# Kernel optimization log

Hardware: AMD Instinct MI355X
Metric: run time of the kernel (lower is better)

## Reference

```python
import jax, jax.numpy as jnp
import numpy as np

IN, H, B, T, OUT = 128, 512, 256, 512, 2

def _lstm_layer(x, Wih, Whh, bih, bhh):
    # x: [B, T, D_in] -> h_seq: [B, T, H]. PyTorch gate order: i, f, g, o.
    gx = jnp.einsum('btd,gd->btg', x, Wih) + bih + bhh  # [B, T, 4H]
    gx = jnp.transpose(gx, (1, 0, 2))                    # [T, B, 4H]
    Hh = Whh.shape[1]
    def step(carry, g_t):
        h, c = carry
        g = g_t + h @ Whh.T
        i = jax.nn.sigmoid(g[:, 0*Hh:1*Hh])
        f = jax.nn.sigmoid(g[:, 1*Hh:2*Hh])
        gg = jnp.tanh(g[:, 2*Hh:3*Hh])
        o = jax.nn.sigmoid(g[:, 3*Hh:4*Hh])
        c = f * c + i * gg
        h = o * jnp.tanh(c)
        return (h, c), h
    h0 = jnp.zeros((x.shape[0], Hh), x.dtype)
    (_, _), hs = jax.lax.scan(step, (h0, h0), gx)
    return jnp.transpose(hs, (1, 0, 2))  # [B, T, H]

def setup_inputs() -> dict:
    key = jax.random.key(0)
    ks = jax.random.split(key, 11)
    s = 1.0 / np.sqrt(H)
    u = lambda k, shp: jax.random.uniform(k, shp, jnp.float32, -s, s)
    return {
        'x':    jax.random.normal(ks[0], (B, T, IN), jnp.float32),
        'Wih0': u(ks[1], (4 * H, IN)), 'Whh0': u(ks[2], (4 * H, H)),
        'bih0': u(ks[3], (4 * H,)),    'bhh0': u(ks[4], (4 * H,)),
        'Wih1': u(ks[5], (4 * H, H)),  'Whh1': u(ks[6], (4 * H, H)),
        'bih1': u(ks[7], (4 * H,)),    'bhh1': u(ks[8], (4 * H,)),
        'Wfc':  u(ks[9], (OUT, H)),    'bfc':  u(ks[10], (OUT,)),
    }

def reference(x, Wih0, Whh0, bih0, bhh0, Wih1, Whh1, bih1, bhh1, Wfc, bfc):
    h1 = _lstm_layer(x, Wih0, Whh0, bih0, bhh0)   # layer 0
    h2 = _lstm_layer(h1, Wih1, Whh1, bih1, bhh1)  # layer 1
    return h2[:, -1, :] @ Wfc.T + bfc             # [B, OUT]
```

## Files before the change

### kernel.cpp

```cpp
#include <hip/hip_runtime.h>

#define IN_DIM 128
#define HID    512
#define BATCH  256
#define SEQT   512
#define G4H    2048
#define K0     640
#define K1     1024
#define NC0    20
#define NC1    32
#define ACOLS  1152
#define ROWB   2304

typedef __attribute__((ext_vector_type(8))) short bf16x8;
typedef __attribute__((ext_vector_type(4))) float f32x4;

#define MFMA16 __builtin_amdgcn_mfma_f32_16x16x32_bf16

__device__ __forceinline__ unsigned short f2bf(float f) {
  unsigned u = __float_as_uint(f);
  u += 0x7fffu + ((u >> 16) & 1u);
  return (unsigned short)(u >> 16);
}
__device__ __forceinline__ float bf2f(unsigned short s) {
  return __uint_as_float(((unsigned)s) << 16);
}
__device__ __forceinline__ float sigm(float x) { return 1.0f / (1.0f + __expf(-x)); }
__device__ __forceinline__ float tanh_f(float x) {
  float xc = fminf(fmaxf(x, -15.0f), 15.0f);
  float e = __expf(2.0f * xc);
  return (e - 1.0f) / (e + 1.0f);
}

__device__ __forceinline__ unsigned ald(const unsigned* p) {
  return __hip_atomic_load(p, __ATOMIC_RELAXED, __HIP_MEMORY_SCOPE_AGENT);
}

__global__ void conv_weights(const float* __restrict__ Wih0, const float* __restrict__ Whh0,
                             const float* __restrict__ Wih1, const float* __restrict__ Whh1,
                             const float* __restrict__ bih0, const float* __restrict__ bhh0,
                             const float* __restrict__ bih1, const float* __restrict__ bhh1,
                             short* __restrict__ W0h, short* __restrict__ W0l,
                             short* __restrict__ W1h, short* __restrict__ W1l,
                             float* __restrict__ bsum0, float* __restrict__ bsum1) {
  int idx = blockIdx.x * blockDim.x + threadIdx.x;
  const int N0 = G4H * K0, N1 = G4H * K1;
  if (idx < N0) {
    int tile = idx / (K0 * 16), rem = idx % (K0 * 16);
    int kcg = rem >> 9, l = (rem >> 3) & 63, j = rem & 7;
    int slice = tile >> 2, g = tile & 3;
    int c = l & 15, k = kcg * 32 + ((l >> 4) << 3) + j;
    int n = g * HID + slice * 16 + c;
    float w = (k < IN_DIM) ? Wih0[n * IN_DIM + k] : Whh0[n * HID + (k - IN_DIM)];
    unsigned short hi = f2bf(w);
    W0h[idx] = (short)hi;
    W0l[idx] = (short)f2bf(w - bf2f(hi));
  } else if (idx < N0 + N1) {
    int d = idx - N0;
    int tile = d / (K1 * 16), rem = d % (K1 * 16);
    int kcg = rem >> 9, l = (rem >> 3) & 63, j = rem & 7;
    int slice = tile >> 2, g = tile & 3;
    int c = l & 15, k = kcg * 32 + ((l >> 4) << 3) + j;
    int n = g * HID + slice * 16 + c;
    float w = (k < HID) ? Wih1[n * HID + k] : Whh1[n * HID + (k - HID)];
    unsigned short hi = f2bf(w);
    W1h[d] = (short)hi;
    W1l[d] = (short)f2bf(w - bf2f(hi));
  } else if (idx < N0 + N1 + G4H) {
    int n = idx - (N0 + N1);
    bsum0[n] = bih0[n] + bhh0[n];
  } else if (idx < N0 + N1 + 2 * G4H) {
    int n = idx - (N0 + N1 + G4H);
    bsum1[n] = bih1[n] + bhh1[n];
  }
}

__device__ __forceinline__ void stage_both(char* AhiB, char* AloB,
                                           const unsigned* __restrict__ h0p,
                                           const unsigned* __restrict__ h2p,
                                           int b0, int tid) {
  const int row = tid >> 5, c32 = tid & 31;
  const unsigned* p0 = h0p + (size_t)(b0 + row) * HID + c32 * 16;
  const unsigned* p2 = h2p + (size_t)(b0 + row) * HID + c32 * 16;
  uint4 v0, v1, v2, v3, w0, w1, w2, w3;
  asm volatile(
      "global_load_dwordx4 %0, %8, off sc0 sc1\n\t"
      "global_load_dwordx4 %1, %8, off offset:16 sc0 sc1\n\t"
      "global_load_dwordx4 %2, %8, off offset:32 sc0 sc1\n\t"
      "global_load_dwordx4 %3, %8, off offset:48 sc0 sc1\n\t"
      "global_load_dwordx4 %4, %9, off sc0 sc1\n\t"
      "global_load_dwordx4 %5, %9, off offset:16 sc0 sc1\n\t"
      "global_load_dwordx4 %6, %9, off offset:32 sc0 sc1\n\t"
      "global_load_dwordx4 %7, %9, off offset:48 sc0 sc1\n\t"
      "s_waitcnt vmcnt(0)"
      : "=&v"(v0), "=&v"(v1), "=&v"(v2), "=&v"(v3),
        "=&v"(w0), "=&v"(w1), "=&v"(w2), "=&v"(w3)
      : "v"(p0), "v"(p2)
      : "memory");

  const int rx = (row & 7) << 4;
  char* bh = AhiB + row * ROWB;
  char* bl = AloB + row * ROWB;
#define PKH(a, b) ((unsigned)((a) & 0xffffu) | (((b) & 0xffffu) << 16))
#define PKL(a, b) (((a) >> 16) | ((b) & 0xffff0000u))
  {
    const int byte0 = (IN_DIM + c32 * 16) * 2;
    int4 h0 = {(int)PKH(v0.x, v0.y), (int)PKH(v0.z, v0.w), (int)PKH(v1.x, v1.y), (int)PKH(v1.z, v1.w)};
    int4 h1 = {(int)PKH(v2.x, v2.y), (int)PKH(v2.z, v2.w), (int)PKH(v3.x, v3.y), (int)PKH(v3.z, v3.w)};
    int4 l0 = {(int)PKL(v0.x, v0.y), (int)PKL(v0.z, v0.w), (int)PKL(v1.x, v1.y), (int)PKL(v1.z, v1.w)};
    int4 l1 = {(int)PKL(v2.x, v2.y), (int)PKL(v2.z, v2.w), (int)PKL(v3.x, v3.y), (int)PKL(v3.z, v3.w)};
    *(int4*)(bh + (byte0 ^ rx)) = h0;
    *(int4*)(bh + ((byte0 + 16) ^ rx)) = h1;
    *(int4*)(bl + (byte0 ^ rx)) = l0;
    *(int4*)(bl + ((byte0 + 16) ^ rx)) = l1;
  }
  {
    const int byte0 = (IN_DIM + HID + c32 * 16) * 2;
    int4 h0 = {(int)PKH(w0.x, w0.y), (int)PKH(w0.z, w0.w), (int)PKH(w1.x, w1.y), (int)PKH(w1.z, w1.w)};
    int4 h1 = {(int)PKH(w2.x, w2.y), (int)PKH(w2.z, w2.w), (int)PKH(w3.x, w3.y), (int)PKH(w3.z, w3.w)};
    int4 l0 = {(int)PKL(w0.x, w0.y), (int)PKL(w0.z, w0.w), (int)PKL(w1.x, w1.y), (int)PKL(w1.z, w1.w)};
    int4 l1 = {(int)PKL(w2.x, w2.y), (int)PKL(w2.z, w2.w), (int)PKL(w3.x, w3.y), (int)PKL(w3.z, w3.w)};
    *(int4*)(bh + (byte0 ^ rx)) = h0;
    *(int4*)(bh + ((byte0 + 16) ^ rx)) = h1;
    *(int4*)(bl + (byte0 ^ rx)) = l0;
    *(int4*)(bl + ((byte0 + 16) ^ rx)) = l1;
  }
#undef PKH
#undef PKL
}

template <int NKC>
__device__ __forceinline__ void gemmq(const char* Ah, const char* Al,
                                      const short* __restrict__ Bh, const short* __restrict__ Bl,
                                      int lane, int aoff, f32x4& acc0, f32x4& acc1) {
  const int row = lane & 15;
  const int ko  = (lane >> 4) * 8;
  const int rx  = (row & 7) << 4;
  const char* pAh0 = Ah + row * ROWB;
  const char* pAh1 = Ah + (row + 16) * ROWB;
  const char* pAl0 = Al + row * ROWB;
  const char* pAl1 = Al + (row + 16) * ROWB;
#pragma unroll
  for (int kc = 0; kc < NKC; ++kc) {
    const int off = ((aoff + kc * 32 + ko) * 2) ^ rx;
    bf16x8 ah0 = *(const bf16x8*)(pAh0 + off);
    bf16x8 ah1 = *(const bf16x8*)(pAh1 + off);
    bf16x8 al0 = *(const bf16x8*)(pAl0 + off);
    bf16x8 al1 = *(const bf16x8*)(pAl1 + off);
    bf16x8 bh  = *(const bf16x8*)(Bh + kc * 512 + lane * 8);
    bf16x8 bl  = *(const bf16x8*)(Bl + kc * 512 + lane * 8);
    acc0 = MFMA16(ah0, bh, acc0, 0, 0, 0);
    acc1 = MFMA16(ah1, bh, acc1, 0, 0, 0);
    acc0 = MFMA16(ah0, bl, acc0, 0, 0, 0);
    acc1 = MFMA16(ah1, bl, acc1, 0, 0, 0);
    acc0 = MFMA16(al0, bh, acc0, 0, 0, 0);
    acc1 = MFMA16(al1, bh, acc1, 0, 0, 0);
  }
}

__device__ __forceinline__ void finq(float* glf, int g, int lane,
                                     const f32x4& a0, const f32x4& a1) {
  const int col = lane & 15;
  const int r0  = (lane >> 4) * 4;
  float* base = glf + g * 512;
#pragma unroll
  for (int r = 0; r < 4; ++r) {
    atomicAdd(base + (r0 + r) * 16 + col, a0[r]);
    atomicAdd(base + (16 + r0 + r) * 16 + col, a1[r]);
  }
}

__device__ __forceinline__ void do_update(float* glf, float& c, const float* bs,
                                          int tid, unsigned (*hbuf)[16]) {
  float gi = glf[tid]        + bs[0];
  float gf = glf[512 + tid]  + bs[1];
  float gg = glf[1024 + tid] + bs[2];
  float go = glf[1536 + tid] + bs[3];
  glf[tid] = 0.f; glf[512 + tid] = 0.f; glf[1024 + tid] = 0.f; glf[1536 + tid] = 0.f;
  float i = sigm(gi), f = sigm(gf), g = tanh_f(gg), o = sigm(go);
  float cc = f * c + i * g;
  c = cc;
  float h = o * tanh_f(cc);
  unsigned short hh = f2bf(h);
  unsigned short hl = f2bf(h - bf2f(hh));
  hbuf[tid >> 4][tid & 15] = (unsigned)hh | ((unsigned)hl << 16);
}

__device__ __forceinline__ void store_h(const unsigned (*hbuf)[16], unsigned* hc,
                                        int b0, int hid0, int tid) {
  if (tid < 128) {
    const int row = tid >> 2, q = tid & 3;
    const unsigned long long* src = (const unsigned long long*)&hbuf[row][q * 4];
    unsigned long long* dst =
        (unsigned long long*)(hc + (size_t)(b0 + row) * HID + hid0 + q * 4);
    __hip_atomic_store(dst, src[0], __ATOMIC_RELAXED, __HIP_MEMORY_SCOPE_AGENT);
    __hip_atomic_store(dst + 1, src[1], __ATOMIC_RELAXED, __HIP_MEMORY_SCOPE_AGENT);
  }
}

__device__ __forceinline__ void group_barrier(unsigned* cnt, unsigned target, int tid) {
  asm volatile("s_waitcnt vmcnt(0)" ::: "memory");
  __syncthreads();
  if (tid == 0) {
    __hip_atomic_fetch_add(cnt, 1u, __ATOMIC_RELAXED, __HIP_MEMORY_SCOPE_AGENT);
    while (__hip_atomic_load(cnt, __ATOMIC_RELAXED, __HIP_MEMORY_SCOPE_AGENT) < target)
      __builtin_amdgcn_s_sleep(1);
  }
  __syncthreads();
}

__global__ void __launch_bounds__(1024, 4) lstm_fused(
    const float* __restrict__ x,
    const float* __restrict__ Wfc, const float* __restrict__ bfc,
    const short* __restrict__ W0h, const short* __restrict__ W0l,
    const short* __restrict__ W1h, const short* __restrict__ W1l,
    const float* __restrict__ bsum0, const float* __restrict__ bsum1,
    unsigned* __restrict__ h0s, unsigned* __restrict__ h2s,
    unsigned* __restrict__ counters,
    float* __restrict__ out) {
  const int tid   = threadIdx.x;
  const int wv    = tid >> 6;
  const int lane  = tid & 63;
  const int slice = blockIdx.x & 31;
  const int grp   = blockIdx.x >> 5;
  const int hid0  = slice * 16;
  const int b0    = grp * 32;
  unsigned* cnt   = counters + grp * 64;

  __shared__ __align__(16) char AhiB[32 * ROWB];
  __shared__ __align__(16) char AloB[32 * ROWB];
  __shared__ float glf[4 * 512];
  __shared__ __align__(16) unsigned hbuf[32][16];

  const int g  = wv & 3;
  const int kq = wv >> 2;
  const short* B0hp = W0h + ((size_t)(slice * 4 + g) * NC0 + (size_t)kq * 5) * 512;
  const short* B0lp = W0l + ((size_t)(slice * 4 + g) * NC0 + (size_t)kq * 5) * 512;
  const short* B1hp = W1h + ((size_t)(slice * 4 + g) * NC1 + (size_t)kq * 8) * 512;
  const short* B1lp = W1l + ((size_t)(slice * 4 + g) * NC1 + (size_t)kq * 8) * 512;
  const int aoff0 = kq * 160;
  const int aoff1 = IN_DIM + kq * 256;

  float c0 = 0.f, c1 = 0.f;
  float bs0[4], bs1[4];
  if (tid < 512) {
    const int n = hid0 + (tid & 15);
#pragma unroll
    for (int q = 0; q < 4; ++q) { bs0[q] = bsum0[q * HID + n]; bs1[q] = bsum1[q * HID + n]; }
    glf[tid] = 0.f; glf[512 + tid] = 0.f; glf[1024 + tid] = 0.f; glf[1536 + tid] = 0.f;
  }

  const size_t PL = (size_t)BATCH * HID;

  for (int s = 0; s <= SEQT; ++s) {
    const int cur = s & 1, prv = cur ^ 1;
    unsigned* h0c = h0s + (size_t)cur * PL;
    const unsigned* h0p = h0s + (size_t)prv * PL;
    unsigned* h2c = h2s + (size_t)cur * PL;
    const unsigned* h2p = h2s + (size_t)prv * PL;

    if (s < SEQT) {
      const int row = tid >> 5, t32 = tid & 31;
      const int rx = (row & 7) << 4;
      const float* xs = x + ((size_t)(b0 + row) * SEQT + s) * IN_DIM + t32 * 4;
      float4 xv = *(const float4*)xs;
      unsigned short h0v = f2bf(xv.x), h1v = f2bf(xv.y), h2v = f2bf(xv.z), h3v = f2bf(xv.w);
      uint2 hd = {(unsigned)h0v | ((unsigned)h1v << 16), (unsigned)h2v | ((unsigned)h3v << 16)};
      uint2 ld = {(unsigned)f2bf(xv.x - bf2f(h0v)) | ((unsigned)f2bf(xv.y - bf2f(h1v)) << 16),
                  (unsigned)f2bf(xv.z - bf2f(h2v)) | ((unsigned)f2bf(xv.w - bf2f(h3v)) << 16)};
      const int byte = (t32 * 8) ^ rx;
      *(uint2*)(AhiB + row * ROWB + byte) = hd;
      *(uint2*)(AloB + row * ROWB + byte) = ld;
    }
    stage_both(AhiB, AloB, h0p, h2p, b0, tid);
    __syncthreads();

    if (s < SEQT) {
      f32x4 a0 = {0.f, 0.f, 0.f, 0.f}, a1 = {0.f, 0.f, 0.f, 0.f};
      gemmq<5>(AhiB, AloB, B0hp, B0lp, lane, aoff0, a0, a1);
      finq(glf, g, lane, a0, a1);
    }
    __syncthreads();
    if (s < SEQT && tid < 512) do_update(glf, c0, bs0, tid, hbuf);
    __syncthreads();

    if (s < SEQT) store_h(hbuf, h0c, b0, hid0, tid);
    if (s > 0) {
      f32x4 a0 = {0.f, 0.f, 0.f, 0.f}, a1 = {0.f, 0.f, 0.f, 0.f};
      gemmq<8>(AhiB, AloB, B1hp, B1lp, lane, aoff1, a0, a1);
      finq(glf, g, lane, a0, a1);
    }
    __syncthreads();
    if (s > 0 && tid < 512) do_update(glf, c1, bs1, tid, hbuf);
    __syncthreads();
    if (s > 0) store_h(hbuf, h2c, b0, hid0, tid);

    group_barrier(cnt, 32u * (unsigned)(s + 1), tid);
  }

  {
    const int p = tid >> 3, q = tid & 7;
    float acc = 0.f;
    if (slice == 0 && tid < 512) {
      const int b = b0 + (p >> 1), o = p & 1;
      const unsigned* sp = h2s + (size_t)b * HID + q * 64;
      const float* wf = Wfc + (size_t)o * HID + q * 64;
#pragma unroll 8
      for (int i = 0; i < 64; ++i) {
        unsigned u = ald(sp + i);
        acc += (bf2f((unsigned short)(u & 0xffff)) + bf2f((unsigned short)(u >> 16))) * wf[i];
      }
      glf[p * 8 + q] = acc;
    }
    __syncthreads();
    if (slice == 0 && tid < 512 && q == 0) {
      float t = 0.f;
#pragma unroll
      for (int i = 0; i < 8; ++i) t += glf[p * 8 + i];
      out[(b0 + (p >> 1)) * 2 + (p & 1)] = t + bfc[p & 1];
    }
  }
}

extern "C" void kernel_launch(void* const* d_in, const int* in_sizes, int n_in,
                              void* d_out, int out_size, void* d_ws, size_t ws_size,
                              hipStream_t stream) {
  const float* x    = (const float*)d_in[0];
  const float* Wih0 = (const float*)d_in[1];
  const float* Whh0 = (const float*)d_in[2];
  const float* bih0 = (const float*)d_in[3];
  const float* bhh0 = (const float*)d_in[4];
  const float* Wih1 = (const float*)d_in[5];
  const float* Whh1 = (const float*)d_in[6];
  const float* bih1 = (const float*)d_in[7];
  const float* bhh1 = (const float*)d_in[8];
  const float* Wfc  = (const float*)d_in[9];
  const float* bfc  = (const float*)d_in[10];
  float* out = (float*)d_out;

  short* W0h = (short*)d_ws;
  short* W0l = W0h + (size_t)G4H * K0;
  short* W1h = W0l + (size_t)G4H * K0;
  short* W1l = W1h + (size_t)G4H * K1;
  unsigned* h0s = (unsigned*)(W1l + (size_t)G4H * K1);
  unsigned* h2s = h0s + (size_t)2 * BATCH * HID;
  unsigned* counters = h2s + (size_t)2 * BATCH * HID;
  float* bsum0 = (float*)(counters + 512);
  float* bsum1 = bsum0 + G4H;

  (void)hipMemsetAsync(h0s, 0,
                       (size_t)4 * BATCH * HID * sizeof(unsigned) + 512 * sizeof(unsigned),
                       stream);

  const int total = G4H * K0 + G4H * K1 + 2 * G4H;
  conv_weights<<<(total + 255) / 256, 256, 0, stream>>>(
      Wih0, Whh0, Wih1, Whh1, bih0, bhh0, bih1, bhh1,
      W0h, W0l, W1h, W1l, bsum0, bsum1);

  void* args[] = {(void*)&x,    (void*)&Wfc,  (void*)&bfc,
                  (void*)&W0h,  (void*)&W0l,  (void*)&W1h, (void*)&W1l,
                  (void*)&bsum0, (void*)&bsum1,
                  (void*)&h0s,  (void*)&h2s,  (void*)&counters, (void*)&out};
  (void)hipLaunchCooperativeKernel((void*)lstm_fused, dim3(256), dim3(1024), args, 0,
                                   stream);
}
```

Baseline: 16.85 ms.

## Split workgroups by LSTM layer so both layers' steps run concurrently

Each workgroup now owns one layer (role from block index) and 32 hidden units, instead of computing both layers serially for 16 units. Per time step this drops from five block barriers with two GEMM/update phases to three barriers with one phase. The GEMM computes two 16-column tiles per wave. The gate buffer gets a padded [row][gate][col] layout, and h is stored directly to global without an LDS staging buffer. The cost is a heavier per-wave MFMA load for the layer-1 role, which now sets the per-step critical path.

```diff
diff --git a/kernel.cpp b/kernel.cpp
--- a/kernel.cpp
+++ b/kernel.cpp
@@ -9,13 +9,13 @@
 #define K1     1024
 #define NC0    20
 #define NC1    32
-#define ACOLS  1152
-#define ROWB   2304
+#define ROWB   2048
 
 typedef __attribute__((ext_vector_type(8))) short bf16x8;
 typedef __attribute__((ext_vector_type(4))) float f32x4;
 
 #define MFMA16 __builtin_amdgcn_mfma_f32_16x16x32_bf16
+#define GL(r, g, c) ((r) * 132 + (g) * 33 + (c))
 
 __device__ __forceinline__ unsigned short f2bf(float f) {
   unsigned u = __float_as_uint(f);
@@ -75,13 +75,48 @@
   }
 }
 
-__device__ __forceinline__ void stage_both(char* AhiB, char* AloB,
-                                           const unsigned* __restrict__ h0p,
-                                           const unsigned* __restrict__ h2p,
-                                           int b0, int tid) {
+#define PKH(a, b) ((unsigned)((a) & 0xffffu) | (((b) & 0xffffu) << 16))
+#define PKL(a, b) (((a) >> 16) | ((b) & 0xffff0000u))
+
+__device__ __forceinline__ void unpack16(char* bh, char* bl, int byte0, int rx,
+                                         const uint4& v0, const uint4& v1,
+                                         const uint4& v2, const uint4& v3) {
+  int4 h0 = {(int)PKH(v0.x, v0.y), (int)PKH(v0.z, v0.w), (int)PKH(v1.x, v1.y), (int)PKH(v1.z, v1.w)};
+  int4 h1 = {(int)PKH(v2.x, v2.y), (int)PKH(v2.z, v2.w), (int)PKH(v3.x, v3.y), (int)PKH(v3.z, v3.w)};
+  int4 l0 = {(int)PKL(v0.x, v0.y), (int)PKL(v0.z, v0.w), (int)PKL(v1.x, v1.y), (int)PKL(v1.z, v1.w)};
+  int4 l1 = {(int)PKL(v2.x, v2.y), (int)PKL(v2.z, v2.w), (int)PKL(v3.x, v3.y), (int)PKL(v3.z, v3.w)};
+  *(int4*)(bh + (byte0 ^ rx)) = h0;
+  *(int4*)(bh + ((byte0 + 16) ^ rx)) = h1;
+  *(int4*)(bl + (byte0 ^ rx)) = l0;
+  *(int4*)(bl + ((byte0 + 16) ^ rx)) = l1;
+}
+
+__device__ __forceinline__ void stage_one(char* AhiB, char* AloB,
+                                          const unsigned* __restrict__ plane,
+                                          int b0, int colOff, int tid) {
   const int row = tid >> 5, c32 = tid & 31;
-  const unsigned* p0 = h0p + (size_t)(b0 + row) * HID + c32 * 16;
-  const unsigned* p2 = h2p + (size_t)(b0 + row) * HID + c32 * 16;
+  const unsigned* p = plane + (size_t)(b0 + row) * HID + c32 * 16;
+  uint4 v0, v1, v2, v3;
+  asm volatile(
+      "global_load_dwordx4 %0, %4, off sc0 sc1\n\t"
+      "global_load_dwordx4 %1, %4, off offset:16 sc0 sc1\n\t"
+      "global_load_dwordx4 %2, %4, off offset:32 sc0 sc1\n\t"
+      "global_load_dwordx4 %3, %4, off offset:48 sc0 sc1\n\t"
+      "s_waitcnt vmcnt(0)"
+      : "=&v"(v0), "=&v"(v1), "=&v"(v2), "=&v"(v3)
+      : "v"(p)
+      : "memory");
+  const int rx = (row & 7) << 4;
+  unpack16(AhiB + row * ROWB, AloB + row * ROWB, (colOff + c32 * 16) * 2, rx, v0, v1, v2, v3);
+}
+
+__device__ __forceinline__ void stage_two(char* AhiB, char* AloB,
+                                          const unsigned* __restrict__ pA,
+                                          const unsigned* __restrict__ pB,
+                                          int b0, int tid) {
+  const int row = tid >> 5, c32 = tid & 31;
+  const unsigned* p0 = pA + (size_t)(b0 + row) * HID + c32 * 16;
+  const unsigned* p2 = pB + (size_t)(b0 + row) * HID + c32 * 16;
   uint4 v0, v1, v2, v3, w0, w1, w2, w3;
   asm volatile(
       "global_load_dwordx4 %0, %8, off sc0 sc1\n\t"
@@ -97,42 +132,21 @@
         "=&v"(w0), "=&v"(w1), "=&v"(w2), "=&v"(w3)
       : "v"(p0), "v"(p2)
       : "memory");
-
   const int rx = (row & 7) << 4;
   char* bh = AhiB + row * ROWB;
   char* bl = AloB + row * ROWB;
-#define PKH(a, b) ((unsigned)((a) & 0xffffu) | (((b) & 0xffffu) << 16))
-#define PKL(a, b) (((a) >> 16) | ((b) & 0xffff0000u))
-  {
-    const int byte0 = (IN_DIM + c32 * 16) * 2;
-    int4 h0 = {(int)PKH(v0.x, v0.y), (int)PKH(v0.z, v0.w), (int)PKH(v1.x, v1.y), (int)PKH(v1.z, v1.w)};
-    int4 h1 = {(int)PKH(v2.x, v2.y), (int)PKH(v2.z, v2.w), (int)PKH(v3.x, v3.y), (int)PKH(v3.z, v3.w)};
-    int4 l0 = {(int)PKL(v0.x, v0.y), (int)PKL(v0.z, v0.w), (int)PKL(v1.x, v1.y), (int)PKL(v1.z, v1.w)};
-    int4 l1 = {(int)PKL(v2.x, v2.y), (int)PKL(v2.z, v2.w), (int)PKL(v3.x, v3.y), (int)PKL(v3.z, v3.w)};
-    *(int4*)(bh + (byte0 ^ rx)) = h0;
-    *(int4*)(bh + ((byte0 + 16) ^ rx)) = h1;
-    *(int4*)(bl + (byte0 ^ rx)) = l0;
-    *(int4*)(bl + ((byte0 + 16) ^ rx)) = l1;
-  }
-  {
-    const int byte0 = (IN_DIM + HID + c32 * 16) * 2;
-    int4 h0 = {(int)PKH(w0.x, w0.y), (int)PKH(w0.z, w0.w), (int)PKH(w1.x, w1.y), (int)PKH(w1.z, w1.w)};
-    int4 h1 = {(int)PKH(w2.x, w2.y), (int)PKH(w2.z, w2.w), (int)PKH(w3.x, w3.y), (int)PKH(w3.z, w3.w)};
-    int4 l0 = {(int)PKL(w0.x, w0.y), (int)PKL(w0.z, w0.w), (int)PKL(w1.x, w1.y), (int)PKL(w1.z, w1.w)};
-    int4 l1 = {(int)PKL(w2.x, w2.y), (int)PKL(w2.z, w2.w), (int)PKL(w3.x, w3.y), (int)PKL(w3.z, w3.w)};
-    *(int4*)(bh + (byte0 ^ rx)) = h0;
-    *(int4*)(bh + ((byte0 + 16) ^ rx)) = h1;
-    *(int4*)(bl + (byte0 ^ rx)) = l0;
-    *(int4*)(bl + ((byte0 + 16) ^ rx)) = l1;
-  }
+  unpack16(bh, bl, (c32 * 16) * 2, rx, v0, v1, v2, v3);
+  unpack16(bh, bl, (HID + c32 * 16) * 2, rx, w0, w1, w2, w3);
+}
 #undef PKH
 #undef PKL
-}
 
 template <int NKC>
-__device__ __forceinline__ void gemmq(const char* Ah, const char* Al,
-                                      const short* __restrict__ Bh, const short* __restrict__ Bl,
-                                      int lane, int aoff, f32x4& acc0, f32x4& acc1) {
+__device__ __forceinline__ void gemm32(const char* Ah, const char* Al,
+                                       const short* __restrict__ Bh0, const short* __restrict__ Bl0,
+                                       const short* __restrict__ Bh1, const short* __restrict__ Bl1,
+                                       int lane, int aoff,
+                                       f32x4& a00, f32x4& a01, f32x4& a10, f32x4& a11) {
   const int row = lane & 15;
   const int ko  = (lane >> 4) * 8;
   const int rx  = (row & 7) << 4;
@@ -147,54 +161,36 @@
     bf16x8 ah1 = *(const bf16x8*)(pAh1 + off);
     bf16x8 al0 = *(const bf16x8*)(pAl0 + off);
     bf16x8 al1 = *(const bf16x8*)(pAl1 + off);
-    bf16x8 bh  = *(const bf16x8*)(Bh + kc * 512 + lane * 8);
-    bf16x8 bl  = *(const bf16x8*)(Bl + kc * 512 + lane * 8);
-    acc0 = MFMA16(ah0, bh, acc0, 0, 0, 0);
-    acc1 = MFMA16(ah1, bh, acc1, 0, 0, 0);
-    acc0 = MFMA16(ah0, bl, acc0, 0, 0, 0);
-    acc1 = MFMA16(ah1, bl, acc1, 0, 0, 0);
-    acc0 = MFMA16(al0, bh, acc0, 0, 0, 0);
-    acc1 = MFMA16(al1, bh, acc1, 0, 0, 0);
-  }
-}
-
-__device__ __forceinline__ void finq(float* glf, int g, int lane,
-                                     const f32x4& a0, const f32x4& a1) {
+    bf16x8 bh0 = *(const bf16x8*)(Bh0 + kc * 512 + lane * 8);
+    bf16x8 bl0 = *(const bf16x8*)(Bl0 + kc * 512 + lane * 8);
+    bf16x8 bh1 = *(const bf16x8*)(Bh1 + kc * 512 + lane * 8);
+    bf16x8 bl1 = *(const bf16x8*)(Bl1 + kc * 512 + lane * 8);
+    a00 = MFMA16(ah0, bh0, a00, 0, 0, 0);
+    a01 = MFMA16(ah1, bh0, a01, 0, 0, 0);
+    a00 = MFMA16(ah0, bl0, a00, 0, 0, 0);
+    a01 = MFMA16(ah1, bl0, a01, 0, 0, 0);
+    a00 = MFMA16(al0, bh0, a00, 0, 0, 0);
+    a01 = MFMA16(al1, bh0, a01, 0, 0, 0);
+    a10 = MFMA16(ah0, bh1, a10, 0, 0, 0);
+    a11 = MFMA16(ah1, bh1, a11, 0, 0, 0);
+    a10 = MFMA16(ah0, bl1, a10, 0, 0, 0);
+    a11 = MFMA16(ah1, bl1, a11, 0, 0, 0);
+    a10 = MFMA16(al0, bh1, a10, 0, 0, 0);
+    a11 = MFMA16(al1, bh1, a11, 0, 0, 0);
+  }
+}
+
+__device__ __forceinline__ void finq32(float* glf, int g, int lane,
+                                       const f32x4& a00, const f32x4& a01,
+                                       const f32x4& a10, const f32x4& a11) {
   const int col = lane & 15;
   const int r0  = (lane >> 4) * 4;
-  float* base = glf + g * 512;
 #pragma unroll
   for (int r = 0; r < 4; ++r) {
-    atomicAdd(base + (r0 + r) * 16 + col, a0[r]);
-    atomicAdd(base + (16 + r0 + r) * 16 + col, a1[r]);
-  }
-}
-
-__device__ __forceinline__ void do_update(float* glf, float& c, const float* bs,
-                                          int tid, unsigned (*hbuf)[16]) {
-  float gi = glf[tid]        + bs[0];
-  float gf = glf[512 + tid]  + bs[1];
-  float gg = glf[1024 + tid] + bs[2];
-  float go = glf[1536 + tid] + bs[3];
-  glf[tid] = 0.f; glf[512 + tid] = 0.f; glf[1024 + tid] = 0.f; glf[1536 + tid] = 0.f;
-  float i = sigm(gi), f = sigm(gf), g = tanh_f(gg), o = sigm(go);
-  float cc = f * c + i * g;
-  c = cc;
-  float h = o * tanh_f(cc);
-  unsigned short hh = f2bf(h);
-  unsigned short hl = f2bf(h - bf2f(hh));
-  hbuf[tid >> 4][tid & 15] = (unsigned)hh | ((unsigned)hl << 16);
-}
-
-__device__ __forceinline__ void store_h(const unsigned (*hbuf)[16], unsigned* hc,
-                                        int b0, int hid0, int tid) {
-  if (tid < 128) {
-    const int row = tid >> 2, q = tid & 3;
-    const unsigned long long* src = (const unsigned long long*)&hbuf[row][q * 4];
-    unsigned long long* dst =
-        (unsigned long long*)(hc + (size_t)(b0 + row) * HID + hid0 + q * 4);
-    __hip_atomic_store(dst, src[0], __ATOMIC_RELAXED, __HIP_MEMORY_SCOPE_AGENT);
-    __hip_atomic_store(dst + 1, src[1], __ATOMIC_RELAXED, __HIP_MEMORY_SCOPE_AGENT);
+    atomicAdd(glf + GL(r0 + r, g, col), a00[r]);
+    atomicAdd(glf + GL(16 + r0 + r, g, col), a01[r]);
+    atomicAdd(glf + GL(r0 + r, g, col + 16), a10[r]);
+    atomicAdd(glf + GL(16 + r0 + r, g, col + 16), a11[r]);
   }
 }
 
@@ -218,37 +214,49 @@
     unsigned* __restrict__ h0s, unsigned* __restrict__ h2s,
     unsigned* __restrict__ counters,
     float* __restrict__ out) {
-  const int tid   = threadIdx.x;
-  const int wv    = tid >> 6;
-  const int lane  = tid & 63;
-  const int slice = blockIdx.x & 31;
-  const int grp   = blockIdx.x >> 5;
-  const int hid0  = slice * 16;
-  const int b0    = grp * 32;
-  unsigned* cnt   = counters + grp * 64;
+  const int tid  = threadIdx.x;
+  const int wv   = tid >> 6;
+  const int lane = tid & 63;
+  const int wid  = blockIdx.x & 31;
+  const int grp  = blockIdx.x >> 5;
+  const int role = wid >> 4;
+  const int w16  = wid & 15;
+  const int hid0 = w16 * 32;
+  const int b0   = grp * 32;
+  unsigned* cnt  = counters + grp * 64;
 
   __shared__ __align__(16) char AhiB[32 * ROWB];
   __shared__ __align__(16) char AloB[32 * ROWB];
-  __shared__ float glf[4 * 512];
-  __shared__ __align__(16) unsigned hbuf[32][16];
+  __shared__ float glf[32 * 132];
 
   const int g  = wv & 3;
   const int kq = wv >> 2;
-  const short* B0hp = W0h + ((size_t)(slice * 4 + g) * NC0 + (size_t)kq * 5) * 512;
-  const short* B0lp = W0l + ((size_t)(slice * 4 + g) * NC0 + (size_t)kq * 5) * 512;
-  const short* B1hp = W1h + ((size_t)(slice * 4 + g) * NC1 + (size_t)kq * 8) * 512;
-  const short* B1lp = W1l + ((size_t)(slice * 4 + g) * NC1 + (size_t)kq * 8) * 512;
-  const int aoff0 = kq * 160;
-  const int aoff1 = IN_DIM + kq * 256;
-
-  float c0 = 0.f, c1 = 0.f;
-  float bs0[4], bs1[4];
-  if (tid < 512) {
-    const int n = hid0 + (tid & 15);
+  const int t0 = (w16 * 2) * 4 + g, t1 = t0 + 4;
+  const short *Bh0, *Bl0, *Bh1, *Bl1;
+  int aoff;
+  if (role == 0) {
+    Bh0 = W0h + ((size_t)t0 * NC0 + (size_t)kq * 5) * 512;
+    Bl0 = W0l + ((size_t)t0 * NC0 + (size_t)kq * 5) * 512;
+    Bh1 = W0h + ((size_t)t1 * NC0 + (size_t)kq * 5) * 512;
+    Bl1 = W0l + ((size_t)t1 * NC0 + (size_t)kq * 5) * 512;
+    aoff = kq * 160;
+  } else {
+    Bh0 = W1h + ((size_t)t0 * NC1 + (size_t)kq * 8) * 512;
+    Bl0 = W1l + ((size_t)t0 * NC1 + (size_t)kq * 8) * 512;
+    Bh1 = W1h + ((size_t)t1 * NC1 + (size_t)kq * 8) * 512;
+    Bl1 = W1l + ((size_t)t1 * NC1 + (size_t)kq * 8) * 512;
+    aoff = kq * 256;
+  }
+
+  float c = 0.f;
+  float bs[4];
+  {
+    const int n = hid0 + (tid & 31);
+    const float* bsp = role ? bsum1 : bsum0;
 #pragma unroll
-    for (int q = 0; q < 4; ++q) { bs0[q] = bsum0[q * HID + n]; bs1[q] = bsum1[q * HID + n]; }
-    glf[tid] = 0.f; glf[512 + tid] = 0.f; glf[1024 + tid] = 0.f; glf[1536 + tid] = 0.f;
-  }
+    for (int q = 0; q < 4; ++q) bs[q] = bsp[q * HID + n];
+  }
+  for (int i = tid; i < 32 * 132; i += 1024) glf[i] = 0.f;
 
   const size_t PL = (size_t)BATCH * HID;
 
@@ -258,42 +266,60 @@
     const unsigned* h0p = h0s + (size_t)prv * PL;
     unsigned* h2c = h2s + (size_t)cur * PL;
     const unsigned* h2p = h2s + (size_t)prv * PL;
-
-    if (s < SEQT) {
-      const int row = tid >> 5, t32 = tid & 31;
-      const int rx = (row & 7) << 4;
-      const float* xs = x + ((size_t)(b0 + row) * SEQT + s) * IN_DIM + t32 * 4;
-      float4 xv = *(const float4*)xs;
-      unsigned short h0v = f2bf(xv.x), h1v = f2bf(xv.y), h2v = f2bf(xv.z), h3v = f2bf(xv.w);
-      uint2 hd = {(unsigned)h0v | ((unsigned)h1v << 16), (unsigned)h2v | ((unsigned)h3v << 16)};
-      uint2 ld = {(unsigned)f2bf(xv.x - bf2f(h0v)) | ((unsigned)f2bf(xv.y - bf2f(h1v)) << 16),
-                  (unsigned)f2bf(xv.z - bf2f(h2v)) | ((unsigned)f2bf(xv.w - bf2f(h3v)) << 16)};
-      const int byte = (t32 * 8) ^ rx;
-      *(uint2*)(AhiB + row * ROWB + byte) = hd;
-      *(uint2*)(AloB + row * ROWB + byte) = ld;
-    }
-    stage_both(AhiB, AloB, h0p, h2p, b0, tid);
+    const bool active = role ? (s > 0) : (s < SEQT);
+
+    if (active) {
+      if (role == 0) {
+        {
+          const int row = tid >> 5, t32 = tid & 31;
+          const int rx = (row & 7) << 4;
+          const float* xs = x + ((size_t)(b0 + row) * SEQT + s) * IN_DIM + t32 * 4;
+          float4 xv = *(const float4*)xs;
+          unsigned short h0v = f2bf(xv.x), h1v = f2bf(xv.y), h2v = f2bf(xv.z), h3v = f2bf(xv.w);
+          uint2 hd = {(unsigned)h0v | ((unsigned)h1v << 16), (unsigned)h2v | ((unsigned)h3v << 16)};
+          uint2 ld = {(unsigned)f2bf(xv.x - bf2f(h0v)) | ((unsigned)f2bf(xv.y - bf2f(h1v)) << 16),
+                      (unsigned)f2bf(xv.z - bf2f(h2v)) | ((unsigned)f2bf(xv.w - bf2f(h3v)) << 16)};
+          const int byte = (t32 * 8) ^ rx;
+          *(uint2*)(AhiB + row * ROWB + byte) = hd;
+          *(uint2*)(AloB + row * ROWB + byte) = ld;
+        }
+        stage_one(AhiB, AloB, h0p, b0, IN_DIM, tid);
+      } else {
+        stage_two(AhiB, AloB, h0p, h2p, b0, tid);
+      }
+    }
     __syncthreads();
 
-    if (s < SEQT) {
-      f32x4 a0 = {0.f, 0.f, 0.f, 0.f}, a1 = {0.f, 0.f, 0.f, 0.f};
-      gemmq<5>(AhiB, AloB, B0hp, B0lp, lane, aoff0, a0, a1);
-      finq(glf, g, lane, a0, a1);
+    if (active) {
+      f32x4 a00 = {0.f, 0.f, 0.f, 0.f}, a01 = {0.f, 0.f, 0.f, 0.f};
+      f32x4 a10 = {0.f, 0.f, 0.f, 0.f}, a11 = {0.f, 0.f, 0.f, 0.f};
+      if (role == 0)
+        gemm32<5>(AhiB, AloB, Bh0, Bl0, Bh1, Bl1, lane, aoff, a00, a01, a10, a11);
+      else
+        gemm32<8>(AhiB, AloB, Bh0, Bl0, Bh1, Bl1, lane, aoff, a00, a01, a10, a11);
+      finq32(glf, g, lane, a00, a01, a10, a11);
     }
     __syncthreads();
-    if (s < SEQT && tid < 512) do_update(glf, c0, bs0, tid, hbuf);
-    __syncthreads();
-
-    if (s < SEQT) store_h(hbuf, h0c, b0, hid0, tid);
-    if (s > 0) {
-      f32x4 a0 = {0.f, 0.f, 0.f, 0.f}, a1 = {0.f, 0.f, 0.f, 0.f};
-      gemmq<8>(AhiB, AloB, B1hp, B1lp, lane, aoff1, a0, a1);
-      finq(glf, g, lane, a0, a1);
-    }
-    __syncthreads();
-    if (s > 0 && tid < 512) do_update(glf, c1, bs1, tid, hbuf);
-    __syncthreads();
-    if (s > 0) store_h(hbuf, h2c, b0, hid0, tid);
+
+    if (active) {
+      const int row = tid >> 5, col = tid & 31;
+      float gi = glf[GL(row, 0, col)] + bs[0];
+      float gf = glf[GL(row, 1, col)] + bs[1];
+      float gg = glf[GL(row, 2, col)] + bs[2];
+      float go = glf[GL(row, 3, col)] + bs[3];
+      glf[GL(row, 0, col)] = 0.f; glf[GL(row, 1, col)] = 0.f;
+      glf[GL(row, 2, col)] = 0.f; glf[GL(row, 3, col)] = 0.f;
+      float i = sigm(gi), f = sigm(gf), gv = tanh_f(gg), o = sigm(go);
+      float cc = f * c + i * gv;
+      c = cc;
+      float h = o * tanh_f(cc);
+      unsigned short hh = f2bf(h);
+      unsigned short hl = f2bf(h - bf2f(hh));
+      unsigned pk = (unsigned)hh | ((unsigned)hl << 16);
+      unsigned* hc = role ? h2c : h0c;
+      __hip_atomic_store(hc + (size_t)(b0 + row) * HID + hid0 + col, pk,
+                         __ATOMIC_RELAXED, __HIP_MEMORY_SCOPE_AGENT);
+    }
 
     group_barrier(cnt, 32u * (unsigned)(s + 1), tid);
   }
@@ -301,7 +327,7 @@
   {
     const int p = tid >> 3, q = tid & 7;
     float acc = 0.f;
-    if (slice == 0 && tid < 512) {
+    if (wid == 0 && tid < 512) {
       const int b = b0 + (p >> 1), o = p & 1;
       const unsigned* sp = h2s + (size_t)b * HID + q * 64;
       const float* wf = Wfc + (size_t)o * HID + q * 64;
@@ -313,7 +339,7 @@
       glf[p * 8 + q] = acc;
     }
     __syncthreads();
-    if (slice == 0 && tid < 512 && q == 0) {
+    if (wid == 0 && tid < 512 && q == 0) {
       float t = 0.f;
 #pragma unroll
       for (int i = 0; i < 8; ++i) t += glf[p * 8 + i];
```

Result: no change. 16.83 ms (-0.1%).
